# Optimization experiments

Measured on AMD Instinct MI355X. Metric: run time of the kernel, lower is better.

Reference implementation:

```python
import jax, jax.numpy as jnp
import numpy as np

D_MODEL = 512
HEADS = 8
HEAD_DIM = D_MODEL // HEADS
TOPK = 16
BIAS_BASE = 1.0
SCALE = 1.0 / np.sqrt(HEAD_DIM)


def setup_inputs() -> dict:
    key = jax.random.key(0)
    ks = jax.random.split(key, 8)
    B, N, T, D = 8, 128, 64, D_MODEL
    h_val = jax.random.normal(ks[0], (B, N, T, D), dtype=jnp.float32)
    h_map = jax.random.normal(ks[1], (B, N, T, D), dtype=jnp.float32)
    base_adj = jax.random.uniform(ks[2], (B, N, N), dtype=jnp.float32)
    std = 0.02
    q_w = jax.random.normal(ks[3], (D, D), dtype=jnp.float32) * std
    k_w = jax.random.normal(ks[4], (D, D), dtype=jnp.float32) * std
    v_w = jax.random.normal(ks[5], (D, D), dtype=jnp.float32) * std
    o_w = jax.random.normal(ks[6], (D, D), dtype=jnp.float32) * std
    # residual_scale parameter: shape [1, N, 1, 1], init 0.5 (clamped to [0,1])
    residual_scale = jnp.full((1, N, 1, 1), 0.5, dtype=jnp.float32)
    return {"h_val": h_val, "h_map": h_map, "base_adj": base_adj,
            "q_w": q_w, "k_w": k_w, "v_w": v_w, "o_w": o_w,
            "residual_scale": residual_scale}


def _topk_mask_scores(scores):
    # scores: [b, h, i, j]; keep top-k per row along j, -inf elsewhere.
    n = scores.shape[-1]
    if TOPK <= 0 or TOPK >= n:
        return scores
    _, idx = jax.lax.top_k(scores, TOPK)              # [b,h,i,k]
    mask = jax.nn.one_hot(idx, n, dtype=jnp.bool_).any(axis=-2)  # [b,h,i,j]
    return jnp.where(mask, scores, -jnp.inf)


def reference(h_val, h_map, base_adj, q_w, k_w, v_w, o_w, residual_scale):
    B, N, T, D = h_val.shape
    # segment summary over tokens
    z_map = h_map.mean(axis=2)                        # [B, N, D]
    # projections (nn.Linear without bias: x @ W.T)
    q = (z_map @ q_w.T).reshape(B, N, HEADS, HEAD_DIM).transpose(0, 2, 1, 3)  # [B,H,N,hd]
    k = (z_map @ k_w.T).reshape(B, N, HEADS, HEAD_DIM).transpose(0, 2, 1, 3)
    scores = jnp.einsum('bhid,bhjd->bhij', q, k) * SCALE
    # log-bias injection from base adjacency
    bias = jnp.log(jnp.clip(base_adj, 1e-12, None))   # [B,N,N]
    scores = scores + BIAS_BASE * bias[:, None]
    raw_attn = jax.nn.softmax(scores, axis=-1)
    attn = jax.nn.softmax(_topk_mask_scores(scores), axis=-1)
    v = (h_val @ v_w.T).reshape(B, N, T, HEADS, HEAD_DIM).transpose(0, 3, 1, 2, 4)  # [B,H,N,T,hd]
    mixed = jnp.einsum('bhij,bhjtd->bhitd', attn, v)  # [B,H,N,T,hd]
    mixed = mixed.transpose(0, 2, 3, 1, 4).reshape(B, N, T, D)
    mixed = mixed @ o_w.T
    scale = jnp.clip(residual_scale, 0.0, 1.0)        # [1,N,1,1]
    out = h_val + mixed * scale                       # dropout is identity (p=0 / eval)
    return out, attn.mean(axis=1), raw_attn.mean(axis=1)
```

## Files before the change

kernel.cpp:

```cpp
#include <hip/hip_runtime.h>
#include <math.h>

#define B_  8
#define N_  128
#define T_  64
#define D_  512
#define H_  8
#define HD_ 64

typedef __attribute__((ext_vector_type(4))) float  f32x4;
typedef __attribute__((ext_vector_type(8))) __bf16 bf16x8;

__device__ __forceinline__ void async_copy16(const void* g, void* l) {
  __builtin_amdgcn_global_load_lds(
      (const __attribute__((address_space(1))) unsigned int*)g,
      (__attribute__((address_space(3))) unsigned int*)l, 16, 0, 0);
}

__global__ __launch_bounds__(256) void zmap_kernel(const float* __restrict__ hmap,
                                                   float* __restrict__ z) {
  __shared__ f32x4 red[128];
  const int bn = blockIdx.x;
  const int c4 = threadIdx.x & 127;
  const int th = threadIdx.x >> 7;
  const float* src = hmap + (size_t)bn * (T_ * D_) + (size_t)th * 32 * D_ + c4 * 4;
  f32x4 s = {0.f, 0.f, 0.f, 0.f};
#pragma unroll 8
  for (int t = 0; t < 32; t++) {
    f32x4 v = *(const f32x4*)&src[(size_t)t * D_];
    s = s + v;
  }
  if (th) red[c4] = s;
  __syncthreads();
  if (!th) {
    f32x4 r = red[c4];
    f32x4 o = (s + r) * (1.f / 64.f);
    *(f32x4*)&z[(size_t)bn * D_ + c4 * 4] = o;
  }
}

__global__ __launch_bounds__(256) void cvt_kernel(const float* __restrict__ s,
                                                  __bf16* __restrict__ d) {
  size_t i = ((size_t)blockIdx.x * 256 + threadIdx.x) << 3;
  f32x4 a = *(const f32x4*)&s[i];
  f32x4 b = *(const f32x4*)&s[i + 4];
  bf16x8 o;
  o[0] = (__bf16)a[0]; o[1] = (__bf16)a[1]; o[2] = (__bf16)a[2]; o[3] = (__bf16)a[3];
  o[4] = (__bf16)b[0]; o[5] = (__bf16)b[1]; o[6] = (__bf16)b[2]; o[7] = (__bf16)b[3];
  *(bf16x8*)&d[i] = o;
}

__global__ __launch_bounds__(256) void qk_gemm(const float* __restrict__ A,
    const float* __restrict__ W, float* __restrict__ Out) {
  __shared__ __bf16 As[64][72];
  __shared__ __bf16 Bs[64][72];
  const int tid  = threadIdx.x;
  const int n0   = blockIdx.x * 64;
  const int m0   = blockIdx.y * 64;
  const int lane = tid & 63, wv = tid >> 6;
  const int quad = lane >> 4, l15 = lane & 15;
  const int sr   = tid >> 2;
  f32x4 acc[4] = {};
  for (int kc = 0; kc < 512; kc += 64) {
#pragma unroll
    for (int i = 0; i < 4; i++) {
      int c = ((tid & 3) << 2) + (i << 4);
      f32x4 v = *(const f32x4*)&A[(size_t)(m0 + sr) * 512 + kc + c];
      As[sr][c + 0] = (__bf16)v[0]; As[sr][c + 1] = (__bf16)v[1];
      As[sr][c + 2] = (__bf16)v[2]; As[sr][c + 3] = (__bf16)v[3];
      f32x4 w = *(const f32x4*)&W[(size_t)(n0 + sr) * 512 + kc + c];
      Bs[sr][c + 0] = (__bf16)w[0]; Bs[sr][c + 1] = (__bf16)w[1];
      Bs[sr][c + 2] = (__bf16)w[2]; Bs[sr][c + 3] = (__bf16)w[3];
    }
    __syncthreads();
#pragma unroll
    for (int ks = 0; ks < 64; ks += 32) {
      bf16x8 a = *(const bf16x8*)&As[(wv << 4) + l15][ks + (quad << 3)];
#pragma unroll
      for (int ct = 0; ct < 4; ct++) {
        bf16x8 b = *(const bf16x8*)&Bs[(ct << 4) + l15][ks + (quad << 3)];
        acc[ct] = __builtin_amdgcn_mfma_f32_16x16x32_bf16(a, b, acc[ct], 0, 0, 0);
      }
    }
    __syncthreads();
  }
#pragma unroll
  for (int ct = 0; ct < 4; ct++)
#pragma unroll
    for (int r = 0; r < 4; r++) {
      const size_t m = (size_t)m0 + (wv << 4) + (quad << 2) + r;
      const size_t n = (size_t)n0 + (ct << 4) + l15;
      Out[m * 512 + n] = acc[ct][r];
    }
}

template<int MODE>
__global__ __launch_bounds__(256) void gemm128(const __bf16* __restrict__ A,
    const float* __restrict__ Af, const __bf16* __restrict__ Wb,
    void* __restrict__ Out, const float* __restrict__ hval,
    const float* __restrict__ rscale) {
  __align__(16) __shared__ __bf16 As[128 * 64];
  __align__(16) __shared__ __bf16 Bs[128 * 64];
  const int tid = threadIdx.x;
  const int lane = tid & 63, wv = tid >> 6;
  const int n0 = blockIdx.x << 7;
  const int m0 = blockIdx.y << 7;
  const int quad = lane >> 4, l15 = lane & 15;
  const int mq = (wv >> 1) << 6, nq = (wv & 1) << 6;
  f32x4 acc[4][4] = {};

  float sc = 0.f;
  if (MODE == 2) sc = fminf(fmaxf(rscale[((m0 + mq) >> 6) & 127], 0.f), 1.f);

  for (int kc = 0; kc < 512; kc += 64) {
    if (MODE == 1) {
#pragma unroll
      for (int it = 0; it < 4; it++) {
        const int gb = (wv << 8) + (it << 6);
        const int s  = gb + lane;
        const int m  = s >> 3, c = (s & 7) ^ (m & 7);
        async_copy16(Wb + (size_t)(n0 + m) * 512 + kc + (c << 3), &Bs[gb << 3]);
      }
#pragma unroll
      for (int it = 0; it < 4; it++) {
        const int s  = (wv << 8) + (it << 6) + lane;
        const int m  = s >> 3, cp = s & 7;
        const float* src = Af + (size_t)(m0 + m) * 512 + kc + (cp << 3);
        f32x4 u0 = *(const f32x4*)src;
        f32x4 u1 = *(const f32x4*)(src + 4);
        bf16x8 o;
        o[0] = (__bf16)u0[0]; o[1] = (__bf16)u0[1];
        o[2] = (__bf16)u0[2]; o[3] = (__bf16)u0[3];
        o[4] = (__bf16)u1[0]; o[5] = (__bf16)u1[1];
        o[6] = (__bf16)u1[2]; o[7] = (__bf16)u1[3];
        *(bf16x8*)&As[((m << 3) + (cp ^ (m & 7))) << 3] = o;
      }
    } else {
#pragma unroll
      for (int it = 0; it < 4; it++) {
        const int gb = (wv << 8) + (it << 6);
        const int s  = gb + lane;
        const int m  = s >> 3, c = (s & 7) ^ (m & 7);
        async_copy16(A  + (size_t)(m0 + m) * 512 + kc + (c << 3), &As[gb << 3]);
        async_copy16(Wb + (size_t)(n0 + m) * 512 + kc + (c << 3), &Bs[gb << 3]);
      }
    }
    __syncthreads();
#pragma unroll
    for (int k0 = 0; k0 < 64; k0 += 32) {
      const int cc = (k0 >> 3) + quad;
      bf16x8 af[4], bfr[4];
#pragma unroll
      for (int mt = 0; mt < 4; mt++) {
        int m = mq + (mt << 4) + l15;
        af[mt] = *(const bf16x8*)&As[((m << 3) + (cc ^ (m & 7))) << 3];
      }
#pragma unroll
      for (int nt = 0; nt < 4; nt++) {
        int n = nq + (nt << 4) + l15;
        bfr[nt] = *(const bf16x8*)&Bs[((n << 3) + (cc ^ (n & 7))) << 3];
      }
#pragma unroll
      for (int mt = 0; mt < 4; mt++)
#pragma unroll
        for (int nt = 0; nt < 4; nt++)
          acc[mt][nt] = __builtin_amdgcn_mfma_f32_16x16x32_bf16(af[mt], bfr[nt],
                                                                acc[mt][nt], 0, 0, 0);
    }
    __syncthreads();
  }

#pragma unroll
  for (int mt = 0; mt < 4; mt++)
#pragma unroll
    for (int nt = 0; nt < 4; nt++)
#pragma unroll
      for (int r = 0; r < 4; r++) {
        const size_t m = (size_t)m0 + mq + (mt << 4) + (quad << 2) + r;
        const size_t n = (size_t)n0 + nq + (nt << 4) + l15;
        float val = acc[mt][nt][r];
        if (MODE == 1) {
          size_t b = m >> 13, j = (m >> 6) & 127, tt = m & 63;
          size_t h = n >> 6, e = n & 63;
          ((__bf16*)Out)[(((b * 8 + h) * 128 + j) * 64 + tt) * 64 + e] = (__bf16)val;
        } else {
          ((float*)Out)[m * 512 + n] = hval[m * 512 + n] + val * sc;
        }
      }
}

__global__ __launch_bounds__(256) void scores_kernel(
    const float* __restrict__ qb, const float* __restrict__ kb,
    const float* __restrict__ adj, __bf16* __restrict__ attnw,
    float* __restrict__ attn_mean, float* __restrict__ raw_mean) {
  __shared__ float  qs[4][64];
  __shared__ __bf16 ks_[128][66];
  const int ig = blockIdx.x, bh = blockIdx.y;
  const int b = bh >> 3, h = bh & 7;
  const int tid = threadIdx.x;
  {
    int r = tid >> 1, cb = (tid & 1) << 5;
    const float* ksrc = kb + ((size_t)(b * 128 + r)) * 512 + h * 64 + cb;
#pragma unroll
    for (int v = 0; v < 8; v++) {
      f32x4 kv = *(const f32x4*)&ksrc[v * 4];
      ks_[r][cb + v * 4 + 0] = (__bf16)kv[0];
      ks_[r][cb + v * 4 + 1] = (__bf16)kv[1];
      ks_[r][cb + v * 4 + 2] = (__bf16)kv[2];
      ks_[r][cb + v * 4 + 3] = (__bf16)kv[3];
    }
  }
  {
    int r = tid >> 6, ln = tid & 63;
    qs[r][ln] = qb[((size_t)(b * 128 + (ig << 2) + r)) * 512 + h * 64 + ln];
  }
  __syncthreads();
  const int wv = tid >> 6, lane = tid & 63;
  const int i = (ig << 2) + wv;
  const int j0 = lane, j1 = lane + 64;
  float s0 = 0.f, s1 = 0.f;
#pragma unroll 16
  for (int e = 0; e < 64; e++) {
    float qe = qs[wv][e];
    s0 += qe * (float)ks_[j0][e];
    s1 += qe * (float)ks_[j1][e];
  }
  const size_t arow = ((size_t)b * 128 + i) * 128;
  s0 = s0 * 0.125f + logf(fmaxf(adj[arow + j0], 1e-12f));
  s1 = s1 * 0.125f + logf(fmaxf(adj[arow + j1], 1e-12f));
  float mx = fmaxf(s0, s1);
#pragma unroll
  for (int off = 32; off; off >>= 1) mx = fmaxf(mx, __shfl_xor(mx, off));
  float e0 = expf(s0 - mx), e1 = expf(s1 - mx);
  float sum = e0 + e1;
#pragma unroll
  for (int off = 32; off; off >>= 1) sum += __shfl_xor(sum, off);
  float inv = 0.125f / sum;
  atomicAdd(&raw_mean[arow + j0], e0 * inv);
  atomicAdd(&raw_mean[arow + j1], e1 * inv);
  float w0 = s0, w1 = s1;
  bool sel0 = false, sel1 = false;
  float m16 = 0.f, denom = 0.f;
  for (int it = 0; it < 16; it++) {
    float v; int idx;
    if (w1 > w0) { v = w1; idx = j1; } else { v = w0; idx = j0; }
#pragma unroll
    for (int off = 32; off; off >>= 1) {
      float ov = __shfl_xor(v, off);
      int   oi = __shfl_xor(idx, off);
      if (ov > v || (ov == v && oi < idx)) { v = ov; idx = oi; }
    }
    if (it == 0) m16 = v;
    denom += expf(v - m16);
    if (idx == j0) { sel0 = true; w0 = -INFINITY; }
    if (idx == j1) { sel1 = true; w1 = -INFINITY; }
  }
  const float invd = 1.f / denom;
  const float p0 = sel0 ? expf(s0 - m16) * invd : 0.f;
  const float p1 = sel1 ? expf(s1 - m16) * invd : 0.f;
  const size_t ab = ((size_t)bh * 128 + i) * 128;
  attnw[ab + j0] = (__bf16)p0;
  attnw[ab + j1] = (__bf16)p1;
  if (sel0) atomicAdd(&attn_mean[arow + j0], p0 * 0.125f);
  if (sel1) atomicAdd(&attn_mean[arow + j1], p1 * 0.125f);
}

__global__ __launch_bounds__(256) void mix_kernel(
    const __bf16* __restrict__ attnw, const __bf16* __restrict__ vbuf,
    __bf16* __restrict__ mixed) {
  __shared__ __bf16 As[128][136];
  __shared__ __bf16 Bt[64][136];
  const int nt = blockIdx.x;
  const int bh = blockIdx.y;
  const int b = bh >> 3, h = bh & 7;
  const int n0 = nt << 6;
  const int tid = threadIdx.x;
  {
    int i = tid >> 1, cb = (tid & 1) << 6;
    const __bf16* src = attnw + ((size_t)bh * 128 + i) * 128 + cb;
#pragma unroll
    for (int v = 0; v < 8; v++)
      *(bf16x8*)&As[i][cb + (v << 3)] = *(const bf16x8*)&src[v << 3];
  }
  {
    int j = tid >> 1, cb = (tid & 1) << 5;
    const __bf16* src = vbuf + ((size_t)bh * 128 + j) * 4096 + n0 + cb;
#pragma unroll
    for (int v = 0; v < 4; v++) {
      bf16x8 x = *(const bf16x8*)&src[v << 3];
#pragma unroll
      for (int u = 0; u < 8; u++) Bt[cb + (v << 3) + u][j] = x[u];
    }
  }
  __syncthreads();
  const int lane = tid & 63, wv = tid >> 6;
  const int quad = lane >> 4, l15 = lane & 15;
  f32x4 acc[2][4] = {};
#pragma unroll
  for (int kk = 0; kk < 128; kk += 32) {
    bf16x8 a0 = *(const bf16x8*)&As[(wv << 5) + l15][kk + (quad << 3)];
    bf16x8 a1 = *(const bf16x8*)&As[(wv << 5) + 16 + l15][kk + (quad << 3)];
#pragma unroll
    for (int ct = 0; ct < 4; ct++) {
      bf16x8 bb = *(const bf16x8*)&Bt[(ct << 4) + l15][kk + (quad << 3)];
      acc[0][ct] = __builtin_amdgcn_mfma_f32_16x16x32_bf16(a0, bb, acc[0][ct], 0, 0, 0);
      acc[1][ct] = __builtin_amdgcn_mfma_f32_16x16x32_bf16(a1, bb, acc[1][ct], 0, 0, 0);
    }
  }
  const int tt = nt;
#pragma unroll
  for (int rt = 0; rt < 2; rt++)
#pragma unroll
    for (int ct = 0; ct < 4; ct++)
#pragma unroll
      for (int r = 0; r < 4; r++) {
        int i = (wv << 5) + (rt << 4) + (quad << 2) + r;
        int e = (ct << 4) + l15;
        mixed[(((size_t)b * 128 + i) * 64 + tt) * 512 + h * 64 + e] =
            (__bf16)acc[rt][ct][r];
      }
}

extern "C" void kernel_launch(void* const* d_in, const int* in_sizes, int n_in,
                              void* d_out, int out_size, void* d_ws, size_t ws_size,
                              hipStream_t stream) {
  (void)in_sizes; (void)n_in; (void)out_size; (void)ws_size;
  const float* h_val = (const float*)d_in[0];
  const float* h_map = (const float*)d_in[1];
  const float* adj   = (const float*)d_in[2];
  const float* q_w   = (const float*)d_in[3];
  const float* k_w   = (const float*)d_in[4];
  const float* v_w   = (const float*)d_in[5];
  const float* o_w   = (const float*)d_in[6];
  const float* rsc   = (const float*)d_in[7];

  char* ws = (char*)d_ws;
  float*  zmap  = (float*)(ws);
  __bf16* vwb   = (__bf16*)(ws);
  __bf16* owb   = (__bf16*)(ws + (512ull << 10));
  float*  qb    = (float*)(ws + (2ull << 20));
  float*  kb    = (float*)(ws + (4ull << 20));
  __bf16* attnw = (__bf16*)(ws + (6ull << 20));
  __bf16* mixed = (__bf16*)(ws + (8ull << 20));
  __bf16* vbuf  = (__bf16*)(ws + (72ull << 20));

  float* out       = (float*)d_out;
  float* attn_mean = out + 33554432ull;
  float* raw_mean  = attn_mean + 131072ull;

  zmap_kernel<<<1024, 256, 0, stream>>>(h_map, zmap);
  qk_gemm<<<dim3(8, 16), 256, 0, stream>>>(zmap, q_w, qb);
  qk_gemm<<<dim3(8, 16), 256, 0, stream>>>(zmap, k_w, kb);
  cvt_kernel<<<128, 256, 0, stream>>>(v_w, vwb);
  cvt_kernel<<<128, 256, 0, stream>>>(o_w, owb);
  hipMemsetAsync(attn_mean, 0, 2ull * 131072ull * sizeof(float), stream);
  scores_kernel<<<dim3(32, 64), 256, 0, stream>>>(qb, kb, adj, attnw, attn_mean, raw_mean);
  gemm128<1><<<dim3(4, 512), 256, 0, stream>>>(nullptr, h_val, vwb, vbuf, nullptr, nullptr);
  mix_kernel<<<dim3(64, 64), 256, 0, stream>>>(attnw, vbuf, mixed);
  gemm128<2><<<dim3(4, 512), 256, 0, stream>>>(mixed, nullptr, owb, d_out, h_val, rsc);
}
```

Measured before the change: 539.0 us.

## Double-buffer gemm128 LDS tiles with 32-wide K steps and prefetch

Restructures the 128x128 bf16 GEMM main loop into a double-buffered pipeline with 32-wide K chunks. Each iteration issues the next chunk's async LDS copies (or fp32 loads for the converting mode) before the current chunk's MFMAs, so there is one barrier per step instead of two. Launch bounds now request 5 or 4 blocks per SM to raise occupancy. The trade-off is twice as many iterations with a smaller swizzle, plus possible register pressure from the occupancy hint.

```diff
diff --git a/kernel.cpp b/kernel.cpp
--- a/kernel.cpp
+++ b/kernel.cpp
@@ -15,6 +15,13 @@
   __builtin_amdgcn_global_load_lds(
       (const __attribute__((address_space(1))) unsigned int*)g,
       (__attribute__((address_space(3))) unsigned int*)l, 16, 0, 0);
+}
+
+__device__ __forceinline__ bf16x8 cvt8(f32x4 a, f32x4 b) {
+  bf16x8 o;
+  o[0] = (__bf16)a[0]; o[1] = (__bf16)a[1]; o[2] = (__bf16)a[2]; o[3] = (__bf16)a[3];
+  o[4] = (__bf16)b[0]; o[5] = (__bf16)b[1]; o[6] = (__bf16)b[2]; o[7] = (__bf16)b[3];
+  return o;
 }
 
 __global__ __launch_bounds__(256) void zmap_kernel(const float* __restrict__ hmap,
@@ -44,10 +51,7 @@
   size_t i = ((size_t)blockIdx.x * 256 + threadIdx.x) << 3;
   f32x4 a = *(const f32x4*)&s[i];
   f32x4 b = *(const f32x4*)&s[i + 4];
-  bf16x8 o;
-  o[0] = (__bf16)a[0]; o[1] = (__bf16)a[1]; o[2] = (__bf16)a[2]; o[3] = (__bf16)a[3];
-  o[4] = (__bf16)b[0]; o[5] = (__bf16)b[1]; o[6] = (__bf16)b[2]; o[7] = (__bf16)b[3];
-  *(bf16x8*)&d[i] = o;
+  *(bf16x8*)&d[i] = cvt8(a, b);
 }
 
 __global__ __launch_bounds__(256) void qk_gemm(const float* __restrict__ A,
@@ -95,12 +99,12 @@
 }
 
 template<int MODE>
-__global__ __launch_bounds__(256) void gemm128(const __bf16* __restrict__ A,
-    const float* __restrict__ Af, const __bf16* __restrict__ Wb,
-    void* __restrict__ Out, const float* __restrict__ hval,
-    const float* __restrict__ rscale) {
-  __align__(16) __shared__ __bf16 As[128 * 64];
-  __align__(16) __shared__ __bf16 Bs[128 * 64];
+__global__ __launch_bounds__(256, MODE == 2 ? 5 : 4) void gemm128(
+    const __bf16* __restrict__ A, const float* __restrict__ Af,
+    const __bf16* __restrict__ Wb, void* __restrict__ Out,
+    const float* __restrict__ hval, const float* __restrict__ rscale) {
+  __align__(16) __shared__ __bf16 As[2][128 * 32];
+  __align__(16) __shared__ __bf16 Bs[2][128 * 32];
   const int tid = threadIdx.x;
   const int lane = tid & 63, wv = tid >> 6;
   const int n0 = blockIdx.x << 7;
@@ -112,60 +116,67 @@
   float sc = 0.f;
   if (MODE == 2) sc = fminf(fmaxf(rscale[((m0 + mq) >> 6) & 127], 0.f), 1.f);
 
-  for (int kc = 0; kc < 512; kc += 64) {
-    if (MODE == 1) {
-#pragma unroll
-      for (int it = 0; it < 4; it++) {
-        const int gb = (wv << 8) + (it << 6);
-        const int s  = gb + lane;
-        const int m  = s >> 3, c = (s & 7) ^ (m & 7);
-        async_copy16(Wb + (size_t)(n0 + m) * 512 + kc + (c << 3), &Bs[gb << 3]);
+  const int s0_ = tid, s1_ = 256 + tid;
+  const int bm0 = s0_ >> 2, bc0 = (s0_ & 3) ^ (bm0 & 3), cp0 = s0_ & 3;
+  const int bm1 = s1_ >> 2, bc1 = (s1_ & 3) ^ (bm1 & 3), cp1 = s1_ & 3;
+  const int gb0 = (wv << 6), gb1 = 256 + (wv << 6);
+
+  {
+    async_copy16(Wb + (size_t)(n0 + bm0) * 512 + (bc0 << 3), &Bs[0][gb0 << 3]);
+    async_copy16(Wb + (size_t)(n0 + bm1) * 512 + (bc1 << 3), &Bs[0][gb1 << 3]);
+    if (MODE == 2) {
+      async_copy16(A + (size_t)(m0 + bm0) * 512 + (bc0 << 3), &As[0][gb0 << 3]);
+      async_copy16(A + (size_t)(m0 + bm1) * 512 + (bc1 << 3), &As[0][gb1 << 3]);
+    } else {
+      const float* p0 = Af + (size_t)(m0 + bm0) * 512 + (cp0 << 3);
+      const float* p1 = Af + (size_t)(m0 + bm1) * 512 + (cp1 << 3);
+      bf16x8 o0 = cvt8(*(const f32x4*)p0, *(const f32x4*)(p0 + 4));
+      bf16x8 o1 = cvt8(*(const f32x4*)p1, *(const f32x4*)(p1 + 4));
+      *(bf16x8*)&As[0][((bm0 << 2) + (cp0 ^ (bm0 & 3))) << 3] = o0;
+      *(bf16x8*)&As[0][((bm1 << 2) + (cp1 ^ (bm1 & 3))) << 3] = o1;
+    }
+  }
+  __syncthreads();
+
+  for (int t = 0; t < 16; t++) {
+    const int cur = t & 1, nxt = cur ^ 1;
+    f32x4 ua00, ua01, ua10, ua11;
+    if (t < 15) {
+      const int kc = (t + 1) << 5;
+      async_copy16(Wb + (size_t)(n0 + bm0) * 512 + kc + (bc0 << 3), &Bs[nxt][gb0 << 3]);
+      async_copy16(Wb + (size_t)(n0 + bm1) * 512 + kc + (bc1 << 3), &Bs[nxt][gb1 << 3]);
+      if (MODE == 2) {
+        async_copy16(A + (size_t)(m0 + bm0) * 512 + kc + (bc0 << 3), &As[nxt][gb0 << 3]);
+        async_copy16(A + (size_t)(m0 + bm1) * 512 + kc + (bc1 << 3), &As[nxt][gb1 << 3]);
+      } else {
+        const float* p0 = Af + (size_t)(m0 + bm0) * 512 + kc + (cp0 << 3);
+        const float* p1 = Af + (size_t)(m0 + bm1) * 512 + kc + (cp1 << 3);
+        ua00 = *(const f32x4*)p0; ua01 = *(const f32x4*)(p0 + 4);
+        ua10 = *(const f32x4*)p1; ua11 = *(const f32x4*)(p1 + 4);
       }
-#pragma unroll
-      for (int it = 0; it < 4; it++) {
-        const int s  = (wv << 8) + (it << 6) + lane;
-        const int m  = s >> 3, cp = s & 7;
-        const float* src = Af + (size_t)(m0 + m) * 512 + kc + (cp << 3);
-        f32x4 u0 = *(const f32x4*)src;
-        f32x4 u1 = *(const f32x4*)(src + 4);
-        bf16x8 o;
-        o[0] = (__bf16)u0[0]; o[1] = (__bf16)u0[1];
-        o[2] = (__bf16)u0[2]; o[3] = (__bf16)u0[3];
-        o[4] = (__bf16)u1[0]; o[5] = (__bf16)u1[1];
-        o[6] = (__bf16)u1[2]; o[7] = (__bf16)u1[3];
-        *(bf16x8*)&As[((m << 3) + (cp ^ (m & 7))) << 3] = o;
-      }
-    } else {
-#pragma unroll
-      for (int it = 0; it < 4; it++) {
-        const int gb = (wv << 8) + (it << 6);
-        const int s  = gb + lane;
-        const int m  = s >> 3, c = (s & 7) ^ (m & 7);
-        async_copy16(A  + (size_t)(m0 + m) * 512 + kc + (c << 3), &As[gb << 3]);
-        async_copy16(Wb + (size_t)(n0 + m) * 512 + kc + (c << 3), &Bs[gb << 3]);
-      }
-    }
-    __syncthreads();
-#pragma unroll
-    for (int k0 = 0; k0 < 64; k0 += 32) {
-      const int cc = (k0 >> 3) + quad;
-      bf16x8 af[4], bfr[4];
-#pragma unroll
-      for (int mt = 0; mt < 4; mt++) {
-        int m = mq + (mt << 4) + l15;
-        af[mt] = *(const bf16x8*)&As[((m << 3) + (cc ^ (m & 7))) << 3];
-      }
-#pragma unroll
-      for (int nt = 0; nt < 4; nt++) {
-        int n = nq + (nt << 4) + l15;
-        bfr[nt] = *(const bf16x8*)&Bs[((n << 3) + (cc ^ (n & 7))) << 3];
-      }
-#pragma unroll
-      for (int mt = 0; mt < 4; mt++)
-#pragma unroll
-        for (int nt = 0; nt < 4; nt++)
-          acc[mt][nt] = __builtin_amdgcn_mfma_f32_16x16x32_bf16(af[mt], bfr[nt],
-                                                                acc[mt][nt], 0, 0, 0);
+    }
+    bf16x8 af[4], bfr[4];
+#pragma unroll
+    for (int nt = 0; nt < 4; nt++) {
+      int n = nq + (nt << 4) + l15;
+      bfr[nt] = *(const bf16x8*)&Bs[cur][((n << 2) + (quad ^ (n & 3))) << 3];
+    }
+#pragma unroll
+    for (int mt = 0; mt < 4; mt++) {
+      int m = mq + (mt << 4) + l15;
+      af[mt] = *(const bf16x8*)&As[cur][((m << 2) + (quad ^ (m & 3))) << 3];
+    }
+#pragma unroll
+    for (int mt = 0; mt < 4; mt++)
+#pragma unroll
+      for (int nt = 0; nt < 4; nt++)
+        acc[mt][nt] = __builtin_amdgcn_mfma_f32_16x16x32_bf16(af[mt], bfr[nt],
+                                                              acc[mt][nt], 0, 0, 0);
+    if (MODE == 1 && t < 15) {
+      bf16x8 o0 = cvt8(ua00, ua01);
+      bf16x8 o1 = cvt8(ua10, ua11);
+      *(bf16x8*)&As[nxt][((bm0 << 2) + (cp0 ^ (bm0 & 3))) << 3] = o0;
+      *(bf16x8*)&As[nxt][((bm1 << 2) + (cp1 ^ (bm1 & 3))) << 3] = o1;
     }
     __syncthreads();
   }
```

Measured after the change: 755.7 us. 1.4x slower.
